# Optimization experiments

Hardware: AMD Instinct MI355X
Metric: run time of the kernel (lower is better)

Reference implementation:

```python
import jax, jax.numpy as jnp
import numpy as np
from jax import lax

UNITS = 64
LAYERS = 4

def _lstm_layer(x, Wx, U, b):
    # x: [B,T,F]; Keras gate order i,f,c,o; activation=relu, recurrent_activation=sigmoid
    B = x.shape[0]
    xz = jnp.einsum('btf,fg->btg', x, Wx) + b  # precompute input projections [B,T,4U]
    def step(carry, xz_t):
        h, c = carry
        z = xz_t + h @ U
        i, f, g, o = jnp.split(z, 4, axis=-1)
        c = jax.nn.sigmoid(f) * c + jax.nn.sigmoid(i) * jax.nn.relu(g)
        h = jax.nn.sigmoid(o) * jax.nn.relu(c)
        return (h, c), h
    h0 = jnp.zeros((B, UNITS), dtype=x.dtype)
    c0 = jnp.zeros((B, UNITS), dtype=x.dtype)
    _, hs = lax.scan(step, (h0, c0), jnp.swapaxes(xz, 0, 1))
    return jnp.swapaxes(hs, 0, 1)  # [B,T,U]

def setup_inputs() -> dict:
    key = jax.random.key(0)
    ks = jax.random.split(key, 1 + 3 * LAYERS + 2)
    B, T, F = 1024, 512, 1
    d = {'x': jax.random.normal(ks[0], (B, T, F), dtype=jnp.float32)}
    fin = F
    for l in range(LAYERS):
        d[f'Wx{l}'] = jax.random.normal(ks[1 + 3 * l], (fin, 4 * UNITS), dtype=jnp.float32) * 0.05
        d[f'U{l}'] = jax.random.normal(ks[2 + 3 * l], (UNITS, 4 * UNITS), dtype=jnp.float32) * 0.05
        d[f'b{l}'] = jnp.zeros((4 * UNITS,), dtype=jnp.float32)
        fin = UNITS
    d['Wd'] = jax.random.normal(ks[-2], (UNITS, 1), dtype=jnp.float32) * 0.05
    d['bd'] = jnp.zeros((1,), dtype=jnp.float32)
    return d

def reference(x, Wx0, U0, b0, Wx1, U1, b1, Wx2, U2, b2, Wx3, U3, b3, Wd, bd):
    # Dropout is identity at inference.
    h = x
    for Wx, U, b in ((Wx0, U0, b0), (Wx1, U1, b1), (Wx2, U2, b2), (Wx3, U3, b3)):
        h = _lstm_layer(h, Wx, U, b)
    h_last = h[:, -1, :]  # return_sequences=False on last LSTM
    return h_last @ Wd + bd  # [B,1]
```

## Files before the change

kernel.cpp:

```cpp
#include <hip/hip_runtime.h>
#include <stdint.h>

#define TT 512

typedef __fp16   f16x8  __attribute__((ext_vector_type(8)));
typedef float    f32x4  __attribute__((ext_vector_type(4)));
typedef __fp16   fp16x2 __attribute__((ext_vector_type(2)));
typedef uint32_t u32x2  __attribute__((ext_vector_type(2)));

__device__ __forceinline__ f32x4 mfma16(f16x8 a, f16x8 b, f32x4 c) {
    return __builtin_amdgcn_mfma_f32_16x16x32_f16(a, b, c, 0, 0, 0);
}
__device__ __forceinline__ uint32_t pkf16(float a, float b) {
    fp16x2 h = __builtin_amdgcn_cvt_pkrtz(a, b);
    return __builtin_bit_cast(uint32_t, h);
}

#define REP8(M) M(0)M(1)M(2)M(3)M(4)M(5)M(6)M(7)

#define GA(SRC, T, F) (f16x8){ \
  (__fp16)(SRC)[(32*(F)+8*quad+0)*256 + 16*(T)+l15], \
  (__fp16)(SRC)[(32*(F)+8*quad+1)*256 + 16*(T)+l15], \
  (__fp16)(SRC)[(32*(F)+8*quad+2)*256 + 16*(T)+l15], \
  (__fp16)(SRC)[(32*(F)+8*quad+3)*256 + 16*(T)+l15], \
  (__fp16)(SRC)[(32*(F)+8*quad+4)*256 + 16*(T)+l15], \
  (__fp16)(SRC)[(32*(F)+8*quad+5)*256 + 16*(T)+l15], \
  (__fp16)(SRC)[(32*(F)+8*quad+6)*256 + 16*(T)+l15], \
  (__fp16)(SRC)[(32*(F)+8*quad+7)*256 + 16*(T)+l15] }

#define DECLT(j) f16x8 uA##j##_0, uA##j##_1, wA##j##_0, wA##j##_1; f32x4 bias##j;
#define LOADT(j) { \
  const int Tg_ = ((j)>>1)*4 + 2*h + ((j)&1); \
  uA##j##_0 = GA(Uw, Tg_, 0); uA##j##_1 = GA(Uw, Tg_, 1); \
  bias##j = (f32x4){ bw_[16*Tg_ + 4*quad + 0], bw_[16*Tg_ + 4*quad + 1], \
                     bw_[16*Tg_ + 4*quad + 2], bw_[16*Tg_ + 4*quad + 3] }; \
  if (l > 0) { wA##j##_0 = GA(Wsrc, Tg_, 0); wA##j##_1 = GA(Wsrc, Tg_, 1); } \
  else { wA##j##_0 = __builtin_bit_cast(f16x8, (f32x4){ \
           Wx0[16*Tg_+4*quad+0], Wx0[16*Tg_+4*quad+1], \
           Wx0[16*Tg_+4*quad+2], Wx0[16*Tg_+4*quad+3] }); \
         wA##j##_1 = wA##j##_0; } }

#define DECLA(j) f32x4 acc##j;
#define MW0(j) acc##j = mfma16(wA##j##_0, xBp0, bias##j);
#define MW1(j) acc##j = mfma16(wA##j##_1, xBp1, acc##j);
#define MX(j)  acc##j = bias##j + __builtin_bit_cast(f32x4, wA##j##_0) * xvp4;
#define MU0(j) acc##j = mfma16(uA##j##_0, hB0, acc##j);
#define MU1(j) acc##j = mfma16(uA##j##_1, hB1, acc##j);

#define GATES(qp, Ai, Af, Ag, Ao, CST, SAVEK, HK) { \
  f32x4 ei_, ef_, eo_; \
  _Pragma("unroll") for (int r_ = 0; r_ < 4; ++r_) { \
    ei_[r_] = __builtin_amdgcn_exp2f(-1.4426950408889634f * Ai[r_]); \
    ef_[r_] = __builtin_amdgcn_exp2f(-1.4426950408889634f * Af[r_]); \
    eo_[r_] = __builtin_amdgcn_exp2f(-1.4426950408889634f * Ao[r_]); \
  } \
  f32x4 si_, sf_, so_; \
  _Pragma("unroll") for (int r_ = 0; r_ < 4; ++r_) { \
    si_[r_] = __builtin_amdgcn_rcpf(1.0f + ei_[r_]); \
    sf_[r_] = __builtin_amdgcn_rcpf(1.0f + ef_[r_]); \
    so_[r_] = __builtin_amdgcn_rcpf(1.0f + eo_[r_]); \
  } \
  const f32x4 z4_ = {0.f, 0.f, 0.f, 0.f}; \
  f32x4 rg_ = __builtin_elementwise_max(Ag, z4_); \
  f32x4 cv_ = sf_ * CST + si_ * rg_; \
  CST = cv_; \
  f32x4 hv_ = so_ * __builtin_elementwise_max(cv_, z4_); \
  u32x2 pv_ = { pkf16(hv_[0], hv_[1]), pkf16(hv_[2], hv_[3]) }; \
  *(u32x2*)(hw_ + 16*(qp)) = pv_; \
  if (SAVEK) HK = hv_; }

__global__ __launch_bounds__(512)
__attribute__((amdgpu_waves_per_eu(2, 2)))
void lstm_pipe(
    const float* __restrict__ x,
    const float* __restrict__ Wx0, const float* __restrict__ U0, const float* __restrict__ b0,
    const float* __restrict__ Wx1, const float* __restrict__ U1, const float* __restrict__ b1,
    const float* __restrict__ Wx2, const float* __restrict__ U2, const float* __restrict__ b2,
    const float* __restrict__ Wx3, const float* __restrict__ U3, const float* __restrict__ b3,
    const float* __restrict__ Wd,  const float* __restrict__ bd,
    float* __restrict__ out)
{
    extern __shared__ uint32_t smem[];
    __fp16* hb16 = (__fp16*)smem;
    float*  xs   = (float*)(smem + 9216);
    float*  red  = (float*)(smem + 17920);

    const int tid  = threadIdx.x;
    const int lane = tid & 63;
    const int l15  = lane & 15;
    const int quad = lane >> 4;
    const int wv   = tid >> 6;
    const int l    = wv >> 1;
    const int h    = wv & 1;
    const int b0i  = blockIdx.x * 16;

    for (int i = tid; i < 9216; i += 512) smem[i] = 0;
    for (int i = tid; i < 16 * TT; i += 512) {
        int row = i >> 9, t_ = i & (TT - 1);
        xs[t_ * 17 + row] = x[(b0i + row) * TT + t_];
    }

    const float* Uw   = (l == 0) ? U0 : (l == 1) ? U1 : (l == 2) ? U2 : U3;
    const float* bw_  = (l == 0) ? b0 : (l == 1) ? b1 : (l == 2) ? b2 : b3;
    const float* Wsrc = (l == 1) ? Wx1 : (l == 2) ? Wx2 : (l == 3) ? Wx3 : U0;

    REP8(DECLT)
    REP8(LOADT)

    f32x4 cst0 = {0,0,0,0}, cst1 = {0,0,0,0};
    f32x4 hK0  = {0,0,0,0}, hK1  = {0,0,0,0};

    __fp16* hb_l  = hb16 + l * 4608;
    const __fp16* hb_in = hb16 + (l > 0 ? (l - 1) * 4608 : 0);

    f16x8 xBp0 = {}, xBp1 = {};
    float xvp = 0.f;

    __syncthreads();

    if (l == 0) xvp = xs[l15];

    for (int s = 0; s < TT + 6; ++s) {
        const int t = s - 2 * l;
        if (t >= 0 && t < TT) {
            const int sr = (t - 1) & 3, sw = t & 3;

            const __fp16* hp_ = hb_l + sr * 1152 + l15 * 72 + 8 * quad;
            f16x8 hB0 = *(const f16x8*)hp_;
            f16x8 hB1 = *(const f16x8*)(hp_ + 32);

            REP8(DECLA)
            if (l > 0) { REP8(MW0) REP8(MW1) }
            else       { f32x4 xvp4 = {xvp, xvp, xvp, xvp}; REP8(MX) }
            REP8(MU0)
            REP8(MU1)

            __fp16* hw_ = hb_l + sw * 1152 + l15 * 72 + 32 * h + 4 * quad;
            const bool sv_ = (l == 3) && (t == TT - 1);
            GATES(0, acc0, acc2, acc4, acc6, cst0, sv_, hK0)
            GATES(1, acc1, acc3, acc5, acc7, cst1, sv_, hK1)

            if (t + 1 < TT) {
                if (l > 0) {
                    const __fp16* xp_ = hb_in + ((t + 1) & 3) * 1152 + l15 * 72 + 8 * quad;
                    xBp0 = *(const f16x8*)xp_;
                    xBp1 = *(const f16x8*)(xp_ + 32);
                } else {
                    xvp = xs[(t + 1) * 17 + l15];
                }
            }
        } else if (t == -1 && l > 0) {
            const __fp16* xp_ = hb_in + l15 * 72 + 8 * quad;
            xBp0 = *(const f16x8*)xp_;
            xBp1 = *(const f16x8*)(xp_ + 32);
        }
        __syncthreads();
    }

    if (l == 3) {
        float p = 0.f;
        #pragma unroll
        for (int r = 0; r < 4; ++r) {
            p += hK0[r] * Wd[32 * h + 4 * quad + r];
            p += hK1[r] * Wd[32 * h + 16 + 4 * quad + r];
        }
        p += __shfl_down(p, 32, 64);
        p += __shfl_down(p, 16, 64);
        if (lane < 16) red[h * 16 + lane] = p;
    }
    __syncthreads();
    if (wv == 6 && lane < 16) out[b0i + lane] = red[lane] + red[16 + lane] + bd[0];
}

extern "C" void kernel_launch(void* const* d_in, const int* in_sizes, int n_in,
                              void* d_out, int out_size, void* d_ws, size_t ws_size,
                              hipStream_t stream) {
    const float* x   = (const float*)d_in[0];
    const float* Wx0 = (const float*)d_in[1];
    const float* U0  = (const float*)d_in[2];
    const float* b0  = (const float*)d_in[3];
    const float* Wx1 = (const float*)d_in[4];
    const float* U1  = (const float*)d_in[5];
    const float* b1  = (const float*)d_in[6];
    const float* Wx2 = (const float*)d_in[7];
    const float* U2  = (const float*)d_in[8];
    const float* b2  = (const float*)d_in[9];
    const float* Wx3 = (const float*)d_in[10];
    const float* U3  = (const float*)d_in[11];
    const float* b3  = (const float*)d_in[12];
    const float* Wd  = (const float*)d_in[13];
    const float* bd  = (const float*)d_in[14];
    float* out = (float*)d_out;

    static const int kLds = 17952 * 4;
    (void)hipFuncSetAttribute((const void*)lstm_pipe,
                              hipFuncAttributeMaxDynamicSharedMemorySize, kLds);
    hipLaunchKernelGGL(lstm_pipe, dim3(64), dim3(512), kLds, stream,
                       x, Wx0, U0, b0, Wx1, U1, b1, Wx2, U2, b2, Wx3, U3, b3,
                       Wd, bd, out);
}
```

Baseline: 711.5 us.

## Split timestep into MFMA and gate phases staggered across layer pairs

Each loop iteration is split into two barrier-separated phases. Layers 0-1 do their matrix products while layers 2-3 compute gate activations, and then they swap. The intent is to overlap MFMA work with transcendental/VALU gate work from different waves sharing a SIMD. This doubles the number of block-wide barriers per timestep and adds an extra pipeline step.

```diff
diff --git a/kernel.cpp b/kernel.cpp
--- a/kernel.cpp
+++ b/kernel.cpp
@@ -40,12 +40,20 @@
            Wx0[16*Tg_+4*quad+2], Wx0[16*Tg_+4*quad+3] }); \
          wA##j##_1 = wA##j##_0; } }
 
-#define DECLA(j) f32x4 acc##j;
 #define MW0(j) acc##j = mfma16(wA##j##_0, xBp0, bias##j);
 #define MW1(j) acc##j = mfma16(wA##j##_1, xBp1, acc##j);
 #define MX(j)  acc##j = bias##j + __builtin_bit_cast(f32x4, wA##j##_0) * xvp4;
 #define MU0(j) acc##j = mfma16(uA##j##_0, hB0, acc##j);
 #define MU1(j) acc##j = mfma16(uA##j##_1, hB1, acc##j);
+
+#define MFMA_SEG(t_) { \
+  const __fp16* hp_ = hb_l + (((t_)-1)&3)*1152 + l15*72 + 8*quad; \
+  f16x8 hB0 = *(const f16x8*)hp_; \
+  f16x8 hB1 = *(const f16x8*)(hp_ + 32); \
+  if (l > 0) { REP8(MW0) REP8(MW1) } \
+  else       { f32x4 xvp4 = {xvp, xvp, xvp, xvp}; REP8(MX) } \
+  REP8(MU0) \
+  REP8(MU1) }
 
 #define GATES(qp, Ai, Af, Ag, Ao, CST, SAVEK, HK) { \
   f32x4 ei_, ef_, eo_; \
@@ -69,9 +77,14 @@
   *(u32x2*)(hw_ + 16*(qp)) = pv_; \
   if (SAVEK) HK = hv_; }
 
+#define GATE_SEG(tg_, SV_) { \
+  __fp16* hw_ = hb_l + ((tg_)&3)*1152 + l15*72 + 32*h + 4*quad; \
+  GATES(0, acc0, acc2, acc4, acc6, cst0, SV_, hK0) \
+  GATES(1, acc1, acc3, acc5, acc7, cst1, SV_, hK1) }
+
 __global__ __launch_bounds__(512)
 __attribute__((amdgpu_waves_per_eu(2, 2)))
-void lstm_pipe(
+void lstm_phase(
     const float* __restrict__ x,
     const float* __restrict__ Wx0, const float* __restrict__ U0, const float* __restrict__ b0,
     const float* __restrict__ Wx1, const float* __restrict__ U1, const float* __restrict__ b1,
@@ -93,6 +106,7 @@
     const int l    = wv >> 1;
     const int h    = wv & 1;
     const int b0i  = blockIdx.x * 16;
+    const bool phA = (l < 2);
 
     for (int i = tid; i < 9216; i += 512) smem[i] = 0;
     for (int i = tid; i < 16 * TT; i += 512) {
@@ -107,6 +121,7 @@
     REP8(DECLT)
     REP8(LOADT)
 
+    f32x4 acc0, acc1, acc2, acc3, acc4, acc5, acc6, acc7;
     f32x4 cst0 = {0,0,0,0}, cst1 = {0,0,0,0};
     f32x4 hK0  = {0,0,0,0}, hK1  = {0,0,0,0};
 
@@ -120,39 +135,40 @@
 
     if (l == 0) xvp = xs[l15];
 
-    for (int s = 0; s < TT + 6; ++s) {
-        const int t = s - 2 * l;
-        if (t >= 0 && t < TT) {
-            const int sr = (t - 1) & 3, sw = t & 3;
-
-            const __fp16* hp_ = hb_l + sr * 1152 + l15 * 72 + 8 * quad;
-            f16x8 hB0 = *(const f16x8*)hp_;
-            f16x8 hB1 = *(const f16x8*)(hp_ + 32);
-
-            REP8(DECLA)
-            if (l > 0) { REP8(MW0) REP8(MW1) }
-            else       { f32x4 xvp4 = {xvp, xvp, xvp, xvp}; REP8(MX) }
-            REP8(MU0)
-            REP8(MU1)
-
-            __fp16* hw_ = hb_l + sw * 1152 + l15 * 72 + 32 * h + 4 * quad;
-            const bool sv_ = (l == 3) && (t == TT - 1);
-            GATES(0, acc0, acc2, acc4, acc6, cst0, sv_, hK0)
-            GATES(1, acc1, acc3, acc5, acc7, cst1, sv_, hK1)
-
-            if (t + 1 < TT) {
+    for (int s = 0; s < TT + 8; ++s) {
+        if (phA) {
+            const int t = s - 2 * l;
+            if (t >= 0 && t < TT) MFMA_SEG(t)
+        } else {
+            const int tm = s - 2 * l;
+            if (tm >= 0 && tm < TT) {
+                const __fp16* xp_ = hb_in + (tm & 3) * 1152 + l15 * 72 + 8 * quad;
+                xBp0 = *(const f16x8*)xp_;
+                xBp1 = *(const f16x8*)(xp_ + 32);
+            }
+            const int tg = s - 1 - 2 * l;
+            if (tg >= 0 && tg < TT) {
+                const bool sv_ = (l == 3) && (tg == TT - 1);
+                GATE_SEG(tg, sv_)
+            }
+        }
+        __syncthreads();
+        if (phA) {
+            const int tn = s + 1 - 2 * l;
+            if (tn >= 0 && tn < TT) {
                 if (l > 0) {
-                    const __fp16* xp_ = hb_in + ((t + 1) & 3) * 1152 + l15 * 72 + 8 * quad;
+                    const __fp16* xp_ = hb_in + (tn & 3) * 1152 + l15 * 72 + 8 * quad;
                     xBp0 = *(const f16x8*)xp_;
                     xBp1 = *(const f16x8*)(xp_ + 32);
                 } else {
-                    xvp = xs[(t + 1) * 17 + l15];
+                    xvp = xs[tn * 17 + l15];
                 }
             }
-        } else if (t == -1 && l > 0) {
-            const __fp16* xp_ = hb_in + l15 * 72 + 8 * quad;
-            xBp0 = *(const f16x8*)xp_;
-            xBp1 = *(const f16x8*)(xp_ + 32);
+            const int t = s - 2 * l;
+            if (t >= 0 && t < TT) GATE_SEG(t, false)
+        } else {
+            const int t = s - 2 * l;
+            if (t >= 0 && t < TT) MFMA_SEG(t)
         }
         __syncthreads();
     }
@@ -193,9 +209,9 @@
     float* out = (float*)d_out;
 
     static const int kLds = 17952 * 4;
-    (void)hipFuncSetAttribute((const void*)lstm_pipe,
+    (void)hipFuncSetAttribute((const void*)lstm_phase,
                               hipFuncAttributeMaxDynamicSharedMemorySize, kLds);
-    hipLaunchKernelGGL(lstm_pipe, dim3(64), dim3(512), kLds, stream,
+    hipLaunchKernelGGL(lstm_phase, dim3(64), dim3(512), kLds, stream,
                        x, Wx0, U0, b0, Wx1, U1, b1, Wx2, U2, b2, Wx3, U3, b3,
                        Wd, bd, out);
 }
```

Result: faster. 692.3 us (-2.7%).
